# Kernel optimization log

Measured on AMD Instinct MI355X. Metric: run time of the kernel, lower is better.

## Reference

```python
import jax, jax.numpy as jnp
import numpy as np

N_NODES = 100000
N_EDGES = 1600000
IN_FEATS = 128
OUT_FEATS = 128


def setup_inputs() -> dict:
    key = jax.random.key(0)
    k1, k2, k3, k4, k5 = jax.random.split(key, 5)
    feat = jax.random.normal(k1, (N_NODES, IN_FEATS), dtype=jnp.float32)
    # He (kaiming) uniform-ish init scale for the weights
    bound = np.sqrt(6.0 / IN_FEATS).astype(np.float32)
    weight_u = jax.random.uniform(k2, (IN_FEATS, OUT_FEATS), jnp.float32, -bound, bound)
    weight_v = jax.random.uniform(k3, (IN_FEATS, OUT_FEATS), jnp.float32, -bound, bound)
    bias = jnp.zeros((OUT_FEATS,), dtype=jnp.float32)
    src = jax.random.randint(k4, (N_EDGES,), 0, N_NODES, dtype=jnp.int32)
    dst = jax.random.randint(k5, (N_EDGES,), 0, N_NODES, dtype=jnp.int32)
    return {"feat": feat, "weight_u": weight_u, "weight_v": weight_v,
            "bias": bias, "src": src, "dst": dst}


def reference(feat, weight_u, weight_v, bias, src, dst):
    n = feat.shape[0]
    # in_feats (128) is not > out_feats (128) -> aggregate first, then matmul
    # m_i = sum_{j in N(i)} h_j  (copy_u + sum over edges)
    agg = jax.ops.segment_sum(feat[src], dst, num_segments=n)  # [N, in_feats]
    rst_u = jnp.matmul(agg, weight_u)                          # [N, out_feats]
    rst_v = jnp.matmul(feat, weight_v)                         # [N, out_feats]
    # in-degree normalization, clamped at 1
    deg = jax.ops.segment_sum(jnp.ones_like(dst, dtype=feat.dtype), dst,
                              num_segments=n)
    norm = 1.0 / jnp.maximum(deg, 1.0)                         # [N]
    out = jax.nn.relu(rst_v + norm[:, None] * rst_u + bias)
    return out
```

## Files before the change

kernel.cpp:

```cpp
#include <hip/hip_runtime.h>
#include <hip/hip_bf16.h>
#include <stdint.h>

#define NN 100000
#define NE 1600000
#define NF 128
#define NTILE ((NN + 63) / 64)
#define B_BKT 1563
#define NB2 128
#define EPB (NE / NB2)
#define NCNT (B_BKT * NB2)
#define SC2A ((NCNT + 255) / 256)

typedef __attribute__((ext_vector_type(8))) __bf16 bf16x8;
typedef __attribute__((ext_vector_type(4))) float floatx4;
typedef __attribute__((ext_vector_type(4))) unsigned short ushortx4;
typedef __attribute__((ext_vector_type(8))) unsigned short ushortx8;

static __device__ __forceinline__ unsigned short f2bf(float x) {
    union { float f; unsigned u; } v; v.f = x;
    unsigned r = v.u + 0x7fffu + ((v.u >> 16) & 1u);
    return (unsigned short)(r >> 16);
}
static __device__ __forceinline__ float bflo(unsigned w) {
    union { unsigned u; float f; } v; v.u = w << 16; return v.f;
}
static __device__ __forceinline__ float bfhi(unsigned w) {
    union { unsigned u; float f; } v; v.u = w & 0xffff0000u; return v.f;
}

__global__ void k_convert(const float* __restrict__ s, unsigned short* __restrict__ d, int n4) {
    int i = blockIdx.x * blockDim.x + threadIdx.x;
    if (i < n4) {
        floatx4 f = __builtin_nontemporal_load((const floatx4*)s + i);
        ushortx4 o;
        o.x = f2bf(f.x); o.y = f2bf(f.y); o.z = f2bf(f.z); o.w = f2bf(f.w);
        ((ushortx4*)d)[i] = o;
    }
}

__global__ void k_prep(const float* __restrict__ wv, const float* __restrict__ wu,
                       unsigned short* __restrict__ w2t) {
    int id = blockIdx.x * 256 + threadIdx.x;
    if (id >= 128 * 32) return;
    int n = id >> 5, kg = id & 31;
    const float* srcm = (kg < 16) ? wv : wu;
    int k0 = (kg & 15) * 8;
    ushortx8 o;
#pragma unroll
    for (int j = 0; j < 8; ++j)
        o[j] = f2bf(srcm[(k0 + j) * 128 + n]);
    int dchunk = n * 32 + (kg ^ (n & 7));
    *(ushortx8*)(w2t + dchunk * 8) = o;
}

__global__ void k_count(const int* __restrict__ dst, int* __restrict__ counts) {
    __shared__ int h[B_BKT];
    int tid = threadIdx.x;
    for (int i = tid; i < B_BKT; i += 256) h[i] = 0;
    __syncthreads();
    int base = blockIdx.x * EPB, end = base + EPB;
    for (int i = base + tid; i < end; i += 256) {
        int d = __builtin_nontemporal_load(&dst[i]);
        atomicAdd(&h[d >> 6], 1);
    }
    __syncthreads();
    for (int i = tid; i < B_BKT; i += 256)
        counts[i * NB2 + blockIdx.x] = h[i];
}

__global__ void k_scan2_a(int* __restrict__ counts, int* __restrict__ bsums) {
    __shared__ int sh[256];
    int i = blockIdx.x * 256 + threadIdx.x;
    int v = (i < NCNT) ? counts[i] : 0;
    sh[threadIdx.x] = v;
    __syncthreads();
    for (int off = 1; off < 256; off <<= 1) {
        int u = (threadIdx.x >= off) ? sh[threadIdx.x - off] : 0;
        __syncthreads();
        sh[threadIdx.x] += u;
        __syncthreads();
    }
    if (i < NCNT) counts[i] = sh[threadIdx.x] - v;
    if (threadIdx.x == 255) bsums[blockIdx.x] = sh[255];
}
__global__ void k_scan2_b(int* __restrict__ bsums) {
    __shared__ int sh[1024];
    int t = threadIdx.x;
    int v = (t < SC2A) ? bsums[t] : 0;
    sh[t] = v;
    __syncthreads();
    for (int off = 1; off < 1024; off <<= 1) {
        int u = (t >= off) ? sh[t - off] : 0;
        __syncthreads();
        sh[t] += u;
        __syncthreads();
    }
    if (t < SC2A) bsums[t] = sh[t] - v;
}
__global__ void k_scan2_c(int* __restrict__ counts, const int* __restrict__ bsums) {
    int i = blockIdx.x * 256 + threadIdx.x;
    if (i < NCNT) counts[i] += bsums[blockIdx.x];
}

__global__ void k_binscatter(const int* __restrict__ src, const int* __restrict__ dst,
                             const int* __restrict__ counts, unsigned* __restrict__ streams) {
    __shared__ int cur[B_BKT];
    int tid = threadIdx.x;
    for (int i = tid; i < B_BKT; i += 256)
        cur[i] = counts[i * NB2 + blockIdx.x];
    __syncthreads();
    int base = blockIdx.x * EPB, end = base + EPB;
    for (int i = base + tid; i < end; i += 256) {
        int d = __builtin_nontemporal_load(&dst[i]);
        int s = __builtin_nontemporal_load(&src[i]);
        int b = d >> 6;
        unsigned packed = ((unsigned)(d & 63) << 17) | (unsigned)s;
        int pos = atomicAdd(&cur[b], 1);
        streams[pos] = packed;
    }
}

__global__ void k_csr(const unsigned* __restrict__ streams,
                      const int* __restrict__ counts,
                      int* __restrict__ offs, int* __restrict__ csr) {
    __shared__ int hist[64];
    __shared__ int nodeoff[65];
    int tid = threadIdx.x;
    int bkt = blockIdx.x;
    int s = counts[bkt * NB2];
    int e = (bkt == B_BKT - 1) ? NE : counts[(bkt + 1) * NB2];
    if (tid < 64) hist[tid] = 0;
    __syncthreads();
    for (int i = s + tid; i < e; i += 256)
        atomicAdd(&hist[streams[i] >> 17], 1);
    __syncthreads();
    if (tid == 0) {
        int run = 0;
#pragma unroll
        for (int n = 0; n < 64; ++n) { nodeoff[n] = run; run += hist[n]; }
        nodeoff[64] = run;
    }
    __syncthreads();
    if (tid < 64) {
        int node = bkt * 64 + tid;
        if (node < NN) offs[node] = s + nodeoff[tid];
        hist[tid] = nodeoff[tid];
    }
    if (bkt == B_BKT - 1 && tid == 0) offs[NN] = NE;
    __syncthreads();
    for (int i = s + tid; i < e; i += 256) {
        unsigned v = streams[i];
        int p = atomicAdd(&hist[v >> 17], 1);
        csr[s + p] = (int)(v & 0x1FFFFu);
    }
}

__global__ void k_aggregate(const unsigned short* __restrict__ featb,
                            const int* __restrict__ offs,
                            const int* __restrict__ csr,
                            unsigned short* __restrict__ aggb) {
    int lane = threadIdx.x & 63;
    int node = blockIdx.x * 4 + (threadIdx.x >> 6);
    if (node >= NN) return;
    int s0 = offs[node], s1 = offs[node + 1];
    float a0 = 0.f, a1 = 0.f;
    for (int base = s0; base < s1; base += 64) {
        int e = (base + lane < s1) ? csr[base + lane] : 0;
        int m = s1 - base; if (m > 64) m = 64;
        int j = 0;
        for (; j + 8 <= m; j += 8) {
            unsigned w0 = *(const unsigned*)(featb + (size_t)__shfl(e, j + 0, 64) * NF + lane * 2);
            unsigned w1 = *(const unsigned*)(featb + (size_t)__shfl(e, j + 1, 64) * NF + lane * 2);
            unsigned w2 = *(const unsigned*)(featb + (size_t)__shfl(e, j + 2, 64) * NF + lane * 2);
            unsigned w3 = *(const unsigned*)(featb + (size_t)__shfl(e, j + 3, 64) * NF + lane * 2);
            unsigned w4 = *(const unsigned*)(featb + (size_t)__shfl(e, j + 4, 64) * NF + lane * 2);
            unsigned w5 = *(const unsigned*)(featb + (size_t)__shfl(e, j + 5, 64) * NF + lane * 2);
            unsigned w6 = *(const unsigned*)(featb + (size_t)__shfl(e, j + 6, 64) * NF + lane * 2);
            unsigned w7 = *(const unsigned*)(featb + (size_t)__shfl(e, j + 7, 64) * NF + lane * 2);
            a0 += bflo(w0) + bflo(w1) + bflo(w2) + bflo(w3)
                + bflo(w4) + bflo(w5) + bflo(w6) + bflo(w7);
            a1 += bfhi(w0) + bfhi(w1) + bfhi(w2) + bfhi(w3)
                + bfhi(w4) + bfhi(w5) + bfhi(w6) + bfhi(w7);
        }
        for (; j < m; ++j) {
            int nn = __shfl(e, j, 64);
            unsigned w = *(const unsigned*)(featb + (size_t)nn * NF + lane * 2);
            a0 += bflo(w); a1 += bfhi(w);
        }
    }
    int dg = s1 - s0; if (dg < 1) dg = 1;
    float scale = 1.0f / (float)dg;
    unsigned outw = ((unsigned)f2bf(a1 * scale) << 16) | (unsigned)f2bf(a0 * scale);
    *(unsigned*)(aggb + (size_t)node * NF + lane * 2) = outw;
}

__global__ __launch_bounds__(256, 2) void k_gemm(
    const unsigned short* __restrict__ featb,
    const unsigned short* __restrict__ aggb,
    const unsigned short* __restrict__ w2t,
    const float* __restrict__ bias,
    float* __restrict__ out) {
    __shared__ unsigned short lds[128 * 256];
    for (int i = threadIdx.x; i < 4096; i += 256) {
        ushortx8 w = *(const ushortx8*)(w2t + i * 8);
        *(ushortx8*)(&lds[i * 8]) = w;
    }
    __syncthreads();

    int lane = threadIdx.x & 63;
    int wave = threadIdx.x >> 6;
    int quad = lane >> 4, l15 = lane & 15;

    float bsv[8];
#pragma unroll
    for (int ct = 0; ct < 8; ++ct) bsv[ct] = bias[ct * 16 + l15];

    for (int t = blockIdx.x; t < NTILE; t += gridDim.x) {
        int rb = t * 64 + wave * 16;
        int arow = rb + l15; if (arow > NN - 1) arow = NN - 1;
        const unsigned short* fr = featb + (size_t)arow * NF;
        const unsigned short* ar = aggb + (size_t)arow * NF;
        bf16x8 a[8];
#pragma unroll
        for (int ks = 0; ks < 4; ++ks) {
            a[ks]     = *(const bf16x8*)(fr + ks * 32 + quad * 8);
            a[4 + ks] = *(const bf16x8*)(ar + ks * 32 + quad * 8);
        }
        floatx4 acc[8];
#pragma unroll
        for (int ct = 0; ct < 8; ++ct) acc[ct] = (floatx4){0.f, 0.f, 0.f, 0.f};
#pragma unroll
        for (int ct = 0; ct < 8; ++ct) {
            int n = ct * 16 + l15;
            int rowoff = n << 8;
            int sw = n & 7;
#pragma unroll
            for (int ks = 0; ks < 8; ++ks) {
                int kg = ks * 4 + quad;
                bf16x8 b = *(const bf16x8*)(&lds[rowoff + ((kg ^ sw) << 3)]);
                acc[ct] = __builtin_amdgcn_mfma_f32_16x16x32_bf16(a[ks], b, acc[ct], 0, 0, 0);
            }
        }
#pragma unroll
        for (int ct = 0; ct < 8; ++ct) {
            int col = ct * 16 + l15;
#pragma unroll
            for (int r = 0; r < 4; ++r) {
                int row = rb + quad * 4 + r;
                if (row < NN) {
                    float v = acc[ct][r] + bsv[ct];
                    out[(size_t)row * NF + col] = v > 0.f ? v : 0.f;
                }
            }
        }
    }
}

extern "C" void kernel_launch(void* const* d_in, const int* in_sizes, int n_in,
                              void* d_out, int out_size, void* d_ws, size_t ws_size,
                              hipStream_t stream) {
    const float* feat = (const float*)d_in[0];
    const float* wu   = (const float*)d_in[1];
    const float* wv   = (const float*)d_in[2];
    const float* bias = (const float*)d_in[3];
    const int* src    = (const int*)d_in[4];
    const int* dst    = (const int*)d_in[5];
    float* out        = (float*)d_out;

    char* ws = (char*)d_ws;
    int* counts           = (int*)(ws + 0);
    int* bsums            = (int*)(ws + 800256);
    int* offs             = (int*)(ws + 804352);
    int* csr              = (int*)(ws + 1204480);
    unsigned short* featb = (unsigned short*)(ws + 7604480);
    unsigned short* aggb  = (unsigned short*)(ws + 33204480);
    unsigned short* w2t   = (unsigned short*)(ws + 58804480);
    unsigned* streams     = (unsigned*)aggb;

    k_convert<<<(NN * NF / 4 + 255) / 256, 256, 0, stream>>>(feat, featb, NN * NF / 4);
    k_prep<<<16, 256, 0, stream>>>(wv, wu, w2t);

    k_count<<<NB2, 256, 0, stream>>>(dst, counts);
    k_scan2_a<<<SC2A, 256, 0, stream>>>(counts, bsums);
    k_scan2_b<<<1, 1024, 0, stream>>>(bsums);
    k_scan2_c<<<SC2A, 256, 0, stream>>>(counts, bsums);
    k_binscatter<<<NB2, 256, 0, stream>>>(src, dst, counts, streams);
    k_csr<<<B_BKT, 256, 0, stream>>>(streams, counts, offs, csr);
    k_aggregate<<<(NN + 3) / 4, 256, 0, stream>>>(featb, offs, csr, aggb);
    k_gemm<<<768, 256, 0, stream>>>(featb, aggb, w2t, bias, out);
}
```

Measured before the change: 314.6 us.

## Gather 16-byte feature rows with four edges per wave and add nontemporal hints

The aggregation kernel now splits each wave into four 16-lane groups. Each group reads a different edge's full bf16 row with 16-byte loads, and the groups are then combined by cross-lane shuffles, replacing the old scheme of 64 lanes each loading 4 bytes of one edge. This aims to raise memory-level parallelism and load width in the gather, which dominates runtime. Nontemporal loads and stores are also added in the convert, aggregate and GEMM kernels, and the output write loop is reordered. These hints may hurt if the feature table would otherwise stay cached in L2.

```diff
diff --git a/kernel.cpp b/kernel.cpp
--- a/kernel.cpp
+++ b/kernel.cpp
@@ -16,6 +16,7 @@
 typedef __attribute__((ext_vector_type(4))) float floatx4;
 typedef __attribute__((ext_vector_type(4))) unsigned short ushortx4;
 typedef __attribute__((ext_vector_type(8))) unsigned short ushortx8;
+typedef __attribute__((ext_vector_type(4))) unsigned int uintx4;
 
 static __device__ __forceinline__ unsigned short f2bf(float x) {
     union { float f; unsigned u; } v; v.f = x;
@@ -35,7 +36,7 @@
         floatx4 f = __builtin_nontemporal_load((const floatx4*)s + i);
         ushortx4 o;
         o.x = f2bf(f.x); o.y = f2bf(f.y); o.z = f2bf(f.z); o.w = f2bf(f.w);
-        ((ushortx4*)d)[i] = o;
+        __builtin_nontemporal_store(o, (ushortx4*)d + i);
     }
 }
 
@@ -163,36 +164,49 @@
     int lane = threadIdx.x & 63;
     int node = blockIdx.x * 4 + (threadIdx.x >> 6);
     if (node >= NN) return;
+    int g = lane >> 4;
+    int l16 = lane & 15;
     int s0 = offs[node], s1 = offs[node + 1];
-    float a0 = 0.f, a1 = 0.f;
-    for (int base = s0; base < s1; base += 64) {
-        int e = (base + lane < s1) ? csr[base + lane] : 0;
-        int m = s1 - base; if (m > 64) m = 64;
-        int j = 0;
-        for (; j + 8 <= m; j += 8) {
-            unsigned w0 = *(const unsigned*)(featb + (size_t)__shfl(e, j + 0, 64) * NF + lane * 2);
-            unsigned w1 = *(const unsigned*)(featb + (size_t)__shfl(e, j + 1, 64) * NF + lane * 2);
-            unsigned w2 = *(const unsigned*)(featb + (size_t)__shfl(e, j + 2, 64) * NF + lane * 2);
-            unsigned w3 = *(const unsigned*)(featb + (size_t)__shfl(e, j + 3, 64) * NF + lane * 2);
-            unsigned w4 = *(const unsigned*)(featb + (size_t)__shfl(e, j + 4, 64) * NF + lane * 2);
-            unsigned w5 = *(const unsigned*)(featb + (size_t)__shfl(e, j + 5, 64) * NF + lane * 2);
-            unsigned w6 = *(const unsigned*)(featb + (size_t)__shfl(e, j + 6, 64) * NF + lane * 2);
-            unsigned w7 = *(const unsigned*)(featb + (size_t)__shfl(e, j + 7, 64) * NF + lane * 2);
-            a0 += bflo(w0) + bflo(w1) + bflo(w2) + bflo(w3)
-                + bflo(w4) + bflo(w5) + bflo(w6) + bflo(w7);
-            a1 += bfhi(w0) + bfhi(w1) + bfhi(w2) + bfhi(w3)
-                + bfhi(w4) + bfhi(w5) + bfhi(w6) + bfhi(w7);
-        }
-        for (; j < m; ++j) {
-            int nn = __shfl(e, j, 64);
-            unsigned w = *(const unsigned*)(featb + (size_t)nn * NF + lane * 2);
-            a0 += bflo(w); a1 += bfhi(w);
-        }
-    }
-    int dg = s1 - s0; if (dg < 1) dg = 1;
-    float scale = 1.0f / (float)dg;
-    unsigned outw = ((unsigned)f2bf(a1 * scale) << 16) | (unsigned)f2bf(a0 * scale);
-    *(unsigned*)(aggb + (size_t)node * NF + lane * 2) = outw;
+    float acc[8];
+#pragma unroll
+    for (int j = 0; j < 8; ++j) acc[j] = 0.f;
+
+    int base = s0 + g;
+    for (; base + 4 < s1; base += 8) {
+        int e0 = __builtin_nontemporal_load(&csr[base]);
+        int e1 = __builtin_nontemporal_load(&csr[base + 4]);
+        uintx4 w0 = *(const uintx4*)(featb + (e0 << 7) + (l16 << 3));
+        uintx4 w1 = *(const uintx4*)(featb + (e1 << 7) + (l16 << 3));
+        acc[0] += bflo(w0.x); acc[1] += bfhi(w0.x);
+        acc[2] += bflo(w0.y); acc[3] += bfhi(w0.y);
+        acc[4] += bflo(w0.z); acc[5] += bfhi(w0.z);
+        acc[6] += bflo(w0.w); acc[7] += bfhi(w0.w);
+        acc[0] += bflo(w1.x); acc[1] += bfhi(w1.x);
+        acc[2] += bflo(w1.y); acc[3] += bfhi(w1.y);
+        acc[4] += bflo(w1.z); acc[5] += bfhi(w1.z);
+        acc[6] += bflo(w1.w); acc[7] += bfhi(w1.w);
+    }
+    if (base < s1) {
+        int e0 = __builtin_nontemporal_load(&csr[base]);
+        uintx4 w0 = *(const uintx4*)(featb + (e0 << 7) + (l16 << 3));
+        acc[0] += bflo(w0.x); acc[1] += bfhi(w0.x);
+        acc[2] += bflo(w0.y); acc[3] += bfhi(w0.y);
+        acc[4] += bflo(w0.z); acc[5] += bfhi(w0.z);
+        acc[6] += bflo(w0.w); acc[7] += bfhi(w0.w);
+    }
+#pragma unroll
+    for (int j = 0; j < 8; ++j) {
+        acc[j] += __shfl_xor(acc[j], 16, 64);
+        acc[j] += __shfl_xor(acc[j], 32, 64);
+    }
+    if (lane < 16) {
+        int dg = s1 - s0; if (dg < 1) dg = 1;
+        float scale = 1.0f / (float)dg;
+        ushortx8 o;
+#pragma unroll
+        for (int j = 0; j < 8; ++j) o[j] = f2bf(acc[j] * scale);
+        __builtin_nontemporal_store(o, (ushortx8*)(aggb + (size_t)node * NF + (l16 << 3)));
+    }
 }
 
 __global__ __launch_bounds__(256, 2) void k_gemm(
@@ -224,8 +238,8 @@
         bf16x8 a[8];
 #pragma unroll
         for (int ks = 0; ks < 4; ++ks) {
-            a[ks]     = *(const bf16x8*)(fr + ks * 32 + quad * 8);
-            a[4 + ks] = *(const bf16x8*)(ar + ks * 32 + quad * 8);
+            a[ks]     = __builtin_nontemporal_load((const bf16x8*)(fr + ks * 32 + quad * 8));
+            a[4 + ks] = __builtin_nontemporal_load((const bf16x8*)(ar + ks * 32 + quad * 8));
         }
         floatx4 acc[8];
 #pragma unroll
@@ -243,14 +257,15 @@
             }
         }
 #pragma unroll
-        for (int ct = 0; ct < 8; ++ct) {
-            int col = ct * 16 + l15;
-#pragma unroll
-            for (int r = 0; r < 4; ++r) {
-                int row = rb + quad * 4 + r;
-                if (row < NN) {
+        for (int r = 0; r < 4; ++r) {
+            int row = rb + quad * 4 + r;
+            if (row < NN) {
+#pragma unroll
+                for (int ct = 0; ct < 8; ++ct) {
+                    int col = ct * 16 + l15;
                     float v = acc[ct][r] + bsv[ct];
-                    out[(size_t)row * NF + col] = v > 0.f ? v : 0.f;
+                    v = v > 0.f ? v : 0.f;
+                    __builtin_nontemporal_store(v, &out[(size_t)row * NF + col]);
                 }
             }
         }
```

New measurement: 328.1 us. +4.3%, slower.
